# Kernel tuning notes

Hardware: AMD Instinct MI355X
Metric: run time of the kernel (lower is better)

The kernel has to match this reference:

```python
import jax, jax.numpy as jnp
import numpy as np

D_WIN = 6
SIGMA = D_WIN / 2.0  # sigma = D/2
EPS = 1e-6


def _ln(x, g, b):
    m = jnp.mean(x, -1, keepdims=True)
    v = jnp.var(x, -1, keepdims=True)
    return (x - m) / jnp.sqrt(v + EPS) * g + b


def _cross_attn(q, kv, Wq, Wkv, Wproj, bproj, nh):
    # standard multi-head cross attention, no qkv bias (qkv_bias=False)
    B, S, C = q.shape
    N = kv.shape[1]
    hd = C // nh
    scale = hd ** -0.5
    qh = (q @ Wq).reshape(B, S, nh, hd).transpose(0, 2, 1, 3) * scale
    kvh = (kv @ Wkv).reshape(B, N, 2, nh, hd).transpose(2, 0, 3, 1, 4)
    k, v = kvh[0], kvh[1]
    attn = jax.nn.softmax(jnp.einsum('bhsd,bhnd->bhsn', qh, k), -1)
    x = jnp.einsum('bhsn,bhnd->bhsd', attn, v).transpose(0, 2, 1, 3).reshape(B, S, C)
    return x @ Wproj + bproj


def setup_inputs() -> dict:
    key = jax.random.key(0)
    ks = jax.random.split(key, 32)
    B, S, C, H, W = 32, 128, 384, 8, 512

    def lin(k, i, o):
        return jax.random.normal(k, (i, o), jnp.float32) * 0.02

    inp = {
        'q': jax.random.normal(ks[0], (B, S, C), jnp.float32),
        'kv': jax.random.normal(ks[1], (B, H * W, C), jnp.float32),
        # main attention linears (qkv_bias=False)
        'Wq': lin(ks[2], C, C),
        'Wkv': lin(ks[3], C, 2 * C),
        'Wproj': lin(ks[4], C, C), 'bproj': jnp.zeros((C,), jnp.float32),
        # position predictor
        'Wp_w': lin(ks[5], C, C), 'Wp_b': jnp.zeros((C,), jnp.float32),
        'vp_w': lin(ks[6], C, 1), 'vp_b': jnp.zeros((1,), jnp.float32),
        'Wqpos': lin(ks[7], C, C), 'bqpos': jnp.zeros((C,), jnp.float32),
        # simplified RCTC decoder projection
        'Wrctc': lin(ks[8], C, C), 'brctc': jnp.zeros((C,), jnp.float32),
        # pt_to_question cross attention (2 heads)
        'ca1_Wq': lin(ks[9], C, C), 'ca1_Wkv': lin(ks[10], C, 2 * C),
        'ca1_Wproj': lin(ks[11], C, C), 'ca1_bproj': jnp.zeros((C,), jnp.float32),
        # pt_to_image cross attention (2 heads)
        'ca2_Wq': lin(ks[12], C, C), 'ca2_Wkv': lin(ks[13], C, 2 * C),
        'ca2_Wproj': lin(ks[14], C, C), 'ca2_bproj': jnp.zeros((C,), jnp.float32),
        # layernorms
        'g_q1': jnp.ones((C,), jnp.float32), 'b_q1': jnp.zeros((C,), jnp.float32),
        'g_kv1': jnp.ones((C,), jnp.float32), 'b_kv1': jnp.zeros((C,), jnp.float32),
        'g_q2': jnp.ones((C,), jnp.float32), 'b_q2': jnp.zeros((C,), jnp.float32),
        'g_kv2': jnp.ones((C,), jnp.float32), 'b_kv2': jnp.zeros((C,), jnp.float32),
        'sz_h': H, 'sz_w': W,
    }
    return inp


def reference(q, kv, Wq, Wkv, Wproj, bproj, Wp_w, Wp_b, vp_w, vp_b, Wqpos, bqpos,
              Wrctc, brctc, ca1_Wq, ca1_Wkv, ca1_Wproj, ca1_bproj,
              ca2_Wq, ca2_Wkv, ca2_Wproj, ca2_bproj,
              g_q1, b_q1, g_kv1, b_kv1, g_q2, b_q2, g_kv2, b_kv2, sz_h, sz_w):
    B, N, C = kv.shape
    S = q.shape[1]
    H, W = sz_h, sz_w
    nh = 1
    hd = C // nh
    scale = hd ** -0.5

    # RCTC decoder (simplified): (B,N,C) -> (B,C,H,W) -> collapse H -> (B,W,C) -> linear
    kv_img = kv.transpose(0, 2, 1).reshape(B, C, H, W)
    dec = kv_img.mean(axis=2).transpose(0, 2, 1)  # (B, W, C)
    dec = dec @ Wrctc + brctc

    qh = (q @ Wq).reshape(B, S, nh, hd).transpose(0, 2, 1, 3) * scale  # (B,nh,S,hd)
    kvh = (dec @ Wkv).reshape(B, W, 2, nh, hd).transpose(2, 0, 3, 1, 4)
    k, v = kvh[0], kvh[1]  # (B,nh,W,hd)

    # position prediction branch
    p = q @ Wqpos + bqpos
    p = _cross_attn(_ln(p, g_q1, b_q1), _ln(q, g_kv1, b_kv1),
                    ca1_Wq, ca1_Wkv, ca1_Wproj, ca1_bproj, 2)
    p = _cross_attn(_ln(p, g_q2, b_q2), _ln(dec, g_kv2, b_kv2),
                    ca2_Wq, ca2_Wkv, ca2_Wproj, ca2_bproj, 2)
    p_t = jax.nn.sigmoid(jnp.tanh(p @ Wp_w + Wp_b) @ vp_w + vp_b) * W  # (B,S,1)

    # Gaussian window mask around predicted position
    idx = jnp.arange(W, dtype=jnp.float32)[None, None, None, :]     # (1,1,1,W)
    pexp = p_t[:, None, :, :]                                        # (B,1,S,1)
    gauss = jnp.exp(-(idx - pexp) ** 2 / (2.0 * SIGMA ** 2))         # (B,1,S,W)

    attn = jnp.einsum('bhsd,bhwd->bhsw', qh, k) * gauss
    attn = jax.nn.softmax(attn, -1)
    x = jnp.einsum('bhsw,bhwd->bhsd', attn, v).transpose(0, 2, 1, 3).reshape(B, S, C)
    return x @ Wproj + bproj
```

## Files before the change

### kernel.cpp

```cpp
#include <hip/hip_runtime.h>
#include <hip/hip_bf16.h>
#include <math.h>

#define B_ 32
#define S_ 128
#define C_ 384
#define H_ 8
#define W_ 512
#define NKV 4096

typedef __attribute__((ext_vector_type(8))) short short8;
typedef __attribute__((ext_vector_type(4))) float floatx4;

static __device__ __forceinline__ ushort f2bf(float v) {
    __hip_bfloat16 h = __float2bfloat16(v);
    return *(ushort*)&h;
}
static __device__ __forceinline__ float ldf(const float* p, size_t i) { return p[i]; }
static __device__ __forceinline__ float ldf(const ushort* p, size_t i) {
    union { uint u; float f; } c; c.u = (uint)p[i] << 16; return c.f;
}

__global__ __launch_bounds__(256) void mean_kernel(const float* __restrict__ kv,
                                                   ushort* __restrict__ dec0b) {
    int v = blockIdx.x * blockDim.x + threadIdx.x;
    int total = B_ * W_ * (C_ / 4);
    if (v >= total) return;
    int c4  = v % (C_ / 4);
    int row = v / (C_ / 4);
    int b = row / W_;
    int w = row % W_;
    const float4* src = (const float4*)kv + (size_t)(b * NKV + w) * (C_ / 4) + c4;
    float4 s = {0.f, 0.f, 0.f, 0.f};
#pragma unroll
    for (int h = 0; h < H_; ++h) {
        float4 t = src[(size_t)h * W_ * (C_ / 4)];
        s.x += t.x; s.y += t.y; s.z += t.z; s.w += t.w;
    }
    ushort4 o;
    o.x = f2bf(s.x * 0.125f); o.y = f2bf(s.y * 0.125f);
    o.z = f2bf(s.z * 0.125f); o.w = f2bf(s.w * 0.125f);
    ((ushort4*)dec0b)[v] = o;
}

__global__ __launch_bounds__(256) void cast_kernel(const float* __restrict__ in,
                                                   ushort* __restrict__ out, int n4) {
    int v = blockIdx.x * blockDim.x + threadIdx.x;
    if (v >= n4) return;
    float4 f = ((const float4*)in)[v];
    ushort4 o;
    o.x = f2bf(f.x); o.y = f2bf(f.y); o.z = f2bf(f.z); o.w = f2bf(f.w);
    ((ushort4*)out)[v] = o;
}

struct WtDesc { const float* src[12]; ushort* dst[12]; int Kd[12]; int Nd[12]; };
__global__ __launch_bounds__(256) void wtcast_kernel(WtDesc d) {
    int wi = blockIdx.y;
    int K = d.Kd[wi], N = d.Nd[wi];
    int tiles_n = N / 32;
    int tile = blockIdx.x;
    if (tile >= (K / 32) * tiles_n) return;
    int k0 = (tile / tiles_n) * 32, n0 = (tile % tiles_n) * 32;
    __shared__ float t[32][33];
    int tid = threadIdx.x;
    int r = tid >> 3, c4 = (tid & 7) * 4;
    float4 v = *(const float4*)&d.src[wi][(size_t)(k0 + r) * N + n0 + c4];
    t[r][c4] = v.x; t[r][c4 + 1] = v.y; t[r][c4 + 2] = v.z; t[r][c4 + 3] = v.w;
    __syncthreads();
    int c = tid >> 3, k4 = (tid & 7) * 4;
    ushort4 o;
    o.x = f2bf(t[k4][c]); o.y = f2bf(t[k4 + 1][c]);
    o.z = f2bf(t[k4 + 2][c]); o.w = f2bf(t[k4 + 3][c]);
    *(ushort4*)&d.dst[wi][(size_t)(n0 + c) * K + k0 + k4] = o;
}

struct GJob {
    const ushort* A; const ushort* Bt;
    const float* bias; float* Cout; ushort* Cbf;
    int M, N, K; float alpha; int act;
};
struct GJobs { GJob j[3]; };

__global__ __launch_bounds__(256) void bgemm_kernel(GJobs gs) {
    const GJob g = gs.j[blockIdx.z];
    const int bm = blockIdx.y * 128, bn = blockIdx.x * 128;
    if (bm >= g.M || bn >= g.N) return;
    __shared__ ushort As[128 * 40];
    __shared__ ushort Bs[128 * 40];
    const int tid = threadIdx.x;
    const int wav = tid >> 6, lane = tid & 63;
    const int wm = (wav >> 1) * 64, wn = (wav & 1) * 64;
    const int lrow = lane & 15, lq = lane >> 4;

    floatx4 acc[4][4] = {};

    const int sr = tid >> 1, sc0 = (tid & 1) * 16;
    const ushort* Ag = g.A + (size_t)(bm + sr) * g.K + sc0;
    const ushort* Bg = g.Bt + (size_t)(bn + sr) * g.K + sc0;
    ushort* Asw = &As[sr * 40 + sc0];
    ushort* Bsw = &Bs[sr * 40 + sc0];

    for (int k0 = 0; k0 < g.K; k0 += 32) {
        uint4 a0 = *(const uint4*)(Ag + k0);
        uint4 a1 = *(const uint4*)(Ag + k0 + 8);
        uint4 b0 = *(const uint4*)(Bg + k0);
        uint4 b1 = *(const uint4*)(Bg + k0 + 8);
        __syncthreads();
        *(uint4*)Asw = a0; *(uint4*)(Asw + 8) = a1;
        *(uint4*)Bsw = b0; *(uint4*)(Bsw + 8) = b1;
        __syncthreads();
        short8 af[4], bfr[4];
#pragma unroll
        for (int i = 0; i < 4; ++i)
            af[i] = *(const short8*)&As[(wm + 16 * i + lrow) * 40 + lq * 8];
#pragma unroll
        for (int j = 0; j < 4; ++j)
            bfr[j] = *(const short8*)&Bs[(wn + 16 * j + lrow) * 40 + lq * 8];
#pragma unroll
        for (int i = 0; i < 4; ++i)
#pragma unroll
            for (int j = 0; j < 4; ++j)
                acc[i][j] = __builtin_amdgcn_mfma_f32_16x16x32_bf16(af[i], bfr[j], acc[i][j], 0, 0, 0);
    }

#pragma unroll
    for (int i = 0; i < 4; ++i)
#pragma unroll
        for (int j = 0; j < 4; ++j) {
            int row = bm + wm + 16 * i + lq * 4;
            int col = bn + wn + 16 * j + lrow;
            float bv = g.bias ? g.bias[col] : 0.f;
#pragma unroll
            for (int r = 0; r < 4; ++r) {
                float v = acc[i][j][r] * g.alpha + bv;
                if (g.act == 1) v = tanhf(v);
                size_t off = (size_t)(row + r) * g.N + col;
                if (g.Cout) g.Cout[off] = v;
                if (g.Cbf) g.Cbf[off] = f2bf(v);
            }
        }
}

static inline void bgemmJ(hipStream_t st, int nj, const GJob* js) {
    GJobs gs;
    int mx = 0, my = 0;
    for (int i = 0; i < nj; ++i) {
        gs.j[i] = js[i];
        int nx = js[i].N / 128, ny = js[i].M / 128;
        if (nx > mx) mx = nx;
        if (ny > my) my = ny;
    }
    for (int i = nj; i < 3; ++i) gs.j[i] = js[0];
    bgemm_kernel<<<dim3(mx, my, nj), 256, 0, st>>>(gs);
}

struct BGArgs {
    const ushort* A; const ushort* Bt;
    const float* bias; float* outF; ushort* outB;
    int lda, ldb, ldo;
    long AsB, BsB, OsB;
    int AsH, BsH, OsH;
    int K, NH;
    float alpha; int act;
};
__global__ __launch_bounds__(256) void battn_kernel(BGArgs g) {
    __shared__ ushort As[64 * 40];
    __shared__ ushort Bs[64 * 40];
    const int bn = blockIdx.x * 64, bm = blockIdx.y * 64;
    const int bat = blockIdx.z, bb = bat / g.NH, hh = bat % g.NH;
    const ushort* A  = g.A  + (size_t)bb * g.AsB + (size_t)hh * g.AsH;
    const ushort* Bt = g.Bt + (size_t)bb * g.BsB + (size_t)hh * g.BsH;
    const int tid = threadIdx.x;
    const int wav = tid >> 6, lane = tid & 63;
    const int lrow = lane & 15, lq = lane >> 4;
    const int sr = tid >> 2, sc0 = (tid & 3) * 8;
    const ushort* Ag = A  + (size_t)(bm + sr) * g.lda + sc0;
    const ushort* Bg = Bt + (size_t)(bn + sr) * g.ldb + sc0;
    ushort* Asw = &As[sr * 40 + sc0];
    ushort* Bsw = &Bs[sr * 40 + sc0];

    floatx4 acc[4] = {};

    for (int k0 = 0; k0 < g.K; k0 += 32) {
        uint4 a = *(const uint4*)(Ag + k0);
        uint4 b = *(const uint4*)(Bg + k0);
        __syncthreads();
        *(uint4*)Asw = a; *(uint4*)Bsw = b;
        __syncthreads();
        short8 af = *(const short8*)&As[(wav * 16 + lrow) * 40 + lq * 8];
#pragma unroll
        for (int j = 0; j < 4; ++j) {
            short8 bf = *(const short8*)&Bs[(16 * j + lrow) * 40 + lq * 8];
            acc[j] = __builtin_amdgcn_mfma_f32_16x16x32_bf16(af, bf, acc[j], 0, 0, 0);
        }
    }

#pragma unroll
    for (int j = 0; j < 4; ++j) {
        int col = bn + 16 * j + lrow;
        float bv = g.bias ? g.bias[col] : 0.f;
        int row0 = bm + wav * 16 + lq * 4;
#pragma unroll
        for (int r = 0; r < 4; ++r) {
            float v = acc[j][r] * g.alpha + bv;
            if (g.act == 1) v = tanhf(v);
            size_t off = (size_t)bb * g.OsB + (size_t)hh * g.OsH
                       + (size_t)(row0 + r) * g.ldo + col;
            if (g.outF) g.outF[off] = v;
            if (g.outB) g.outB[off] = f2bf(v);
        }
    }
}

static inline void battn(hipStream_t st, const ushort* A, const ushort* Bt,
                         const float* bias, float* outF, ushort* outB,
                         int M, int N, int K, float alpha, int act,
                         int lda, long AsB, int AsH,
                         int ldb, long BsB, int BsH,
                         int ldo, long OsB, int OsH,
                         int NH, int nbat) {
    BGArgs g;
    g.A = A; g.Bt = Bt; g.bias = bias; g.outF = outF; g.outB = outB;
    g.lda = lda; g.ldb = ldb; g.ldo = ldo;
    g.AsB = AsB; g.BsB = BsB; g.OsB = OsB;
    g.AsH = AsH; g.BsH = BsH; g.OsH = OsH;
    g.K = K; g.NH = NH; g.alpha = alpha; g.act = act;
    dim3 grid(N / 64, M / 64, nbat);
    battn_kernel<<<grid, 256, 0, st>>>(g);
}

static inline void bgemm64(hipStream_t st, const ushort* A, const ushort* Bt,
                           const float* bias, float* outF, ushort* outB,
                           int M, int N, int K, float alpha, int act) {
    battn(st, A, Bt, bias, outF, outB, M, N, K, alpha, act,
          K, 0, 0, K, 0, 0, N, 0, 0, 1, 1);
}

struct Ln2Desc {
    const void* X0; const float* g0; const float* b0; ushort* Y0; int bf0; int rows0;
    const void* X1; const float* g1; const float* b1; ushort* Y1; int bf1;
};
__global__ __launch_bounds__(128) void ln2_kernel(Ln2Desc d) {
    int row = blockIdx.x;
    const void* X; const float* g; const float* bb; ushort* Y; int isbf;
    if (row < d.rows0) { X = d.X0; g = d.g0; bb = d.b0; Y = d.Y0; isbf = d.bf0; }
    else { row -= d.rows0; X = d.X1; g = d.g1; bb = d.b1; Y = d.Y1; isbf = d.bf1; }
    const float*  xf = (const float*)X + (size_t)row * C_;
    const ushort* xb = (const ushort*)X + (size_t)row * C_;
    ushort* y = Y + (size_t)row * C_;
    int t = threadIdx.x;
    float v0, v1, v2;
    if (isbf) { v0 = ldf(xb, t); v1 = ldf(xb, t + 128); v2 = ldf(xb, t + 256); }
    else      { v0 = ldf(xf, t); v1 = ldf(xf, t + 128); v2 = ldf(xf, t + 256); }
    float s = v0 + v1 + v2, sq = v0 * v0 + v1 * v1 + v2 * v2;
    __shared__ float rs[128], rq[128];
    rs[t] = s; rq[t] = sq; __syncthreads();
    if (t < 64) {
        s = rs[t] + rs[t + 64]; sq = rq[t] + rq[t + 64];
        for (int o = 32; o; o >>= 1) { s += __shfl_down(s, o); sq += __shfl_down(sq, o); }
        if (t == 0) { rs[0] = s; rq[0] = sq; }
    }
    __syncthreads();
    float mean = rs[0] * (1.0f / C_);
    float var  = rq[0] * (1.0f / C_) - mean * mean;
    float inv  = rsqrtf(var + 1e-6f);
    y[t]       = f2bf((v0 - mean) * inv * g[t]       + bb[t]);
    y[t + 128] = f2bf((v1 - mean) * inv * g[t + 128] + bb[t + 128]);
    y[t + 256] = f2bf((v2 - mean) * inv * g[t + 256] + bb[t + 256]);
}

template <int NW, int GAUSS>
__global__ __launch_bounds__(256) void softmax_kernel(
    const float* __restrict__ sc, const float* __restrict__ ptv,
    ushort* __restrict__ P)
{
    int row = blockIdx.x * 4 + (threadIdx.x >> 6);
    int lane = threadIdx.x & 63;
    const float* s = sc + (size_t)row * NW;
    float pcen = GAUSS ? ptv[row] : 0.f;
    float vals[NW / 64];
    float m = -1e30f;
#pragma unroll
    for (int i = 0; i < NW / 64; ++i) {
        int w = lane + 64 * i;
        float v = s[w];
        if (GAUSS) { float dw = (float)w - pcen; v *= expf(dw * dw * (-1.0f / 18.0f)); }
        vals[i] = v; m = fmaxf(m, v);
    }
#pragma unroll
    for (int o = 32; o; o >>= 1) m = fmaxf(m, __shfl_xor(m, o));
    float sum = 0.f;
#pragma unroll
    for (int i = 0; i < NW / 64; ++i) { vals[i] = expf(vals[i] - m); sum += vals[i]; }
#pragma unroll
    for (int o = 32; o; o >>= 1) sum += __shfl_xor(sum, o);
    float rinv = 1.0f / sum;
    ushort* op = P + (size_t)row * NW;
#pragma unroll
    for (int i = 0; i < NW / 64; ++i) op[lane + 64 * i] = f2bf(vals[i] * rinv);
}

__global__ __launch_bounds__(256) void vtrans_kernel(
    const ushort* __restrict__ kvb, ushort* __restrict__ vt,
    int Nw, int C2, int CC)
{
    int b = blockIdx.z;
    int w0 = blockIdx.x * 32, c0 = blockIdx.y * 32;
    __shared__ ushort t[32][33];
    int tid = threadIdx.x;
    int wl = tid >> 3, c4 = (tid & 7) * 4;
    ushort4 v = *(const ushort4*)&kvb[((size_t)b * Nw + w0 + wl) * C2 + CC + c0 + c4];
    t[wl][c4] = v.x; t[wl][c4 + 1] = v.y; t[wl][c4 + 2] = v.z; t[wl][c4 + 3] = v.w;
    __syncthreads();
    int dl = tid >> 3, w4 = (tid & 7) * 4;
    ushort4 o;
    o.x = t[w4][dl]; o.y = t[w4 + 1][dl]; o.z = t[w4 + 2][dl]; o.w = t[w4 + 3][dl];
    *(ushort4*)&vt[((size_t)b * CC + c0 + dl) * Nw + w0 + w4] = o;
}

__global__ __launch_bounds__(128) void pt_kernel(const float* __restrict__ T,
    const float* __restrict__ vpw, const float* __restrict__ vpb,
    float* __restrict__ out) {
    int row = blockIdx.x;
    int t = threadIdx.x;
    const float* x = T + (size_t)row * C_;
    float s = x[t] * vpw[t] + x[t + 128] * vpw[t + 128] + x[t + 256] * vpw[t + 256];
    __shared__ float red[128];
    red[t] = s; __syncthreads();
    if (t < 64) {
        s = red[t] + red[t + 64];
        for (int o = 32; o; o >>= 1) s += __shfl_down(s, o);
        if (t == 0) {
            float z = s + vpb[0];
            out[row] = 512.0f / (1.0f + expf(-z));
        }
    }
}

extern "C" void kernel_launch(void* const* d_in, const int* in_sizes, int n_in,
                              void* d_out, int out_size, void* d_ws, size_t ws_size,
                              hipStream_t stream) {
    const float* q     = (const float*)d_in[0];
    const float* kv    = (const float*)d_in[1];
    const float* Wq    = (const float*)d_in[2];
    const float* Wkv   = (const float*)d_in[3];
    const float* Wproj = (const float*)d_in[4];
    const float* bproj = (const float*)d_in[5];
    const float* Wp_w  = (const float*)d_in[6];
    const float* Wp_b  = (const float*)d_in[7];
    const float* vp_w  = (const float*)d_in[8];
    const float* vp_b  = (const float*)d_in[9];
    const float* Wqpos = (const float*)d_in[10];
    const float* bqpos = (const float*)d_in[11];
    const float* Wrctc = (const float*)d_in[12];
    const float* brctc = (const float*)d_in[13];
    const float* ca1_Wq    = (const float*)d_in[14];
    const float* ca1_Wkv   = (const float*)d_in[15];
    const float* ca1_Wproj = (const float*)d_in[16];
    const float* ca1_bproj = (const float*)d_in[17];
    const float* ca2_Wq    = (const float*)d_in[18];
    const float* ca2_Wkv   = (const float*)d_in[19];
    const float* ca2_Wproj = (const float*)d_in[20];
    const float* ca2_bproj = (const float*)d_in[21];
    const float* g_q1  = (const float*)d_in[22];
    const float* b_q1  = (const float*)d_in[23];
    const float* g_kv1 = (const float*)d_in[24];
    const float* b_kv1 = (const float*)d_in[25];
    const float* g_q2  = (const float*)d_in[26];
    const float* b_q2  = (const float*)d_in[27];
    const float* g_kv2 = (const float*)d_in[28];
    const float* b_kv2 = (const float*)d_in[29];
    float* out = (float*)d_out;
    float* ws  = (float*)d_ws;

    ushort* dec0b = (ushort*)(ws);
    ushort* wb    = (ushort*)(ws + 3145728);
    ushort* qb    = (ushort*)(ws + 4251648);
    ushort* decb  = (ushort*)(ws + 5038080);
    ushort* qhb   = (ushort*)(ws + 8183808);
    float*  p     = ws + 8970240;
    ushort* pb    = (ushort*)(ws + 10543104);
    float*  t1    = ws + 11329536;
    ushort* t1b   = (ushort*)(ws + 12902400);
    ushort* t2b   = (ushort*)(ws + 13688832);
    ushort* qpb   = (ushort*)(ws + 16834560);
    ushort* kvb   = (ushort*)(ws + 17620992);
    ushort* vt    = (ushort*)(ws + 23912448);
    float*  sc    = ws + 27058176;
    ushort* Pb    = (ushort*)(ws + 31252480);
    ushort* xb    = (ushort*)(ws + 33349632);
    float*  ptb   = ws + 34136064;

    ushort* wbWq     = wb;
    ushort* wbWqpos  = wb + 147456;
    ushort* wbWrctc  = wb + 294912;
    ushort* wbC1Wq   = wb + 442368;
    ushort* wbC1Wp   = wb + 589824;
    ushort* wbC2Wq   = wb + 737280;
    ushort* wbC2Wp   = wb + 884736;
    ushort* wbWpw    = wb + 1032192;
    ushort* wbWproj  = wb + 1179648;
    ushort* wbWkv    = wb + 1327104;
    ushort* wbC1Wkv  = wb + 1622016;
    ushort* wbC2Wkv  = wb + 1916928;

    const float rs384 = 0.05103103630798288f;
    const float rs192 = 0.07216878364870323f;

    mean_kernel<<<(B_ * W_ * (C_ / 4) + 255) / 256, 256, 0, stream>>>(kv, dec0b);
    {
        WtDesc d;
        const float* s_[12] = {Wq, Wqpos, Wrctc, ca1_Wq, ca1_Wproj, ca2_Wq, ca2_Wproj,
                               Wp_w, Wproj, Wkv, ca1_Wkv, ca2_Wkv};
        ushort* t_[12] = {wbWq, wbWqpos, wbWrctc, wbC1Wq, wbC1Wp, wbC2Wq, wbC2Wp,
                          wbWpw, wbWproj, wbWkv, wbC1Wkv, wbC2Wkv};
        for (int i = 0; i < 12; ++i) {
            d.src[i] = s_[i]; d.dst[i] = t_[i];
            d.Kd[i] = 384; d.Nd[i] = (i >= 9) ? 768 : 384;
        }
        dim3 grid(288, 12);
        wtcast_kernel<<<grid, 256, 0, stream>>>(d);
        cast_kernel<<<(393216 + 255) / 256, 256, 0, stream>>>(q, qb, 393216);
    }
    {
        GJob js[3];
        js[0] = {dec0b, wbWrctc, brctc, nullptr, decb, B_ * W_, 384, 384, 1.f, 0};
        js[1] = {qb, wbWq, nullptr, nullptr, qhb, B_ * S_, 384, 384, rs384, 0};
        js[2] = {qb, wbWqpos, bqpos, p, nullptr, B_ * S_, 384, 384, 1.f, 0};
        bgemmJ(stream, 3, js);
    }
    {
        Ln2Desc d;
        d.X0 = p; d.g0 = g_q1;  d.b0 = b_q1;  d.Y0 = t1b; d.bf0 = 0; d.rows0 = B_ * S_;
        d.X1 = q; d.g1 = g_kv1; d.b1 = b_kv1; d.Y1 = t2b; d.bf1 = 0;
        ln2_kernel<<<2 * B_ * S_, 128, 0, stream>>>(d);
    }
    {
        GJob js[2];
        js[0] = {t1b, wbC1Wq, nullptr, nullptr, qpb, B_ * S_, 384, 384, rs192, 0};
        js[1] = {t2b, wbC1Wkv, nullptr, nullptr, kvb, B_ * S_, 768, 384, 1.f, 0};
        bgemmJ(stream, 2, js);
    }
    {
        dim3 gt(S_ / 32, C_ / 32, B_);
        vtrans_kernel<<<gt, 256, 0, stream>>>(kvb, vt, S_, 768, 384);
    }
    battn(stream, qpb, kvb, nullptr, sc, nullptr, 128, 128, 192, 1.f, 0,
          384, (long)S_ * 384, 192,
          768, (long)S_ * 768, 192,
          128, (long)2 * S_ * 128, S_ * 128, 2, 64);
    softmax_kernel<128, 0><<<(B_ * 2 * S_) / 4, 256, 0, stream>>>(sc, nullptr, Pb);
    battn(stream, Pb, vt, nullptr, nullptr, xb, 128, 192, 128, 1.f, 0,
          128, (long)2 * S_ * 128, S_ * 128,
          128, (long)C_ * S_, 192 * S_,
          384, (long)S_ * 384, 192, 2, 64);
    bgemm64(stream, xb, wbC1Wp, ca1_bproj, p, nullptr, B_ * S_, 384, 384, 1.f, 0);
    {
        Ln2Desc d;
        d.X0 = p;    d.g0 = g_q2;  d.b0 = b_q2;  d.Y0 = t1b; d.bf0 = 0; d.rows0 = B_ * S_;
        d.X1 = decb; d.g1 = g_kv2; d.b1 = b_kv2; d.Y1 = t2b; d.bf1 = 1;
        ln2_kernel<<<B_ * S_ + B_ * W_, 128, 0, stream>>>(d);
    }
    {
        GJob js[2];
        js[0] = {t1b, wbC2Wq, nullptr, nullptr, qpb, B_ * S_, 384, 384, rs192, 0};
        js[1] = {t2b, wbC2Wkv, nullptr, nullptr, kvb, B_ * W_, 768, 384, 1.f, 0};
        bgemmJ(stream, 2, js);
    }
    {
        dim3 gt(W_ / 32, C_ / 32, B_);
        vtrans_kernel<<<gt, 256, 0, stream>>>(kvb, vt, W_, 768, 384);
    }
    battn(stream, qpb, kvb, nullptr, sc, nullptr, 128, 512, 192, 1.f, 0,
          384, (long)S_ * 384, 192,
          768, (long)W_ * 768, 192,
          512, (long)2 * S_ * 512, S_ * 512, 2, 64);
    softmax_kernel<512, 0><<<(B_ * 2 * S_) / 4, 256, 0, stream>>>(sc, nullptr, Pb);
    battn(stream, Pb, vt, nullptr, nullptr, xb, 128, 192, 512, 1.f, 0,
          512, (long)2 * S_ * 512, S_ * 512,
          512, (long)C_ * W_, 192 * W_,
          384, (long)S_ * 384, 192, 2, 64);
    bgemm64(stream, xb, wbC2Wp, ca2_bproj, p, pb, B_ * S_, 384, 384, 1.f, 0);
    {
        GJob js[2];
        js[0] = {pb, wbWpw, Wp_b, t1, nullptr, B_ * S_, 384, 384, 1.f, 1};
        js[1] = {decb, wbWkv, nullptr, nullptr, kvb, B_ * W_, 768, 384, 1.f, 0};
        bgemmJ(stream, 2, js);
    }
    pt_kernel<<<B_ * S_, 128, 0, stream>>>(t1, vp_w, vp_b, ptb);
    {
        dim3 gt(W_ / 32, C_ / 32, B_);
        vtrans_kernel<<<gt, 256, 0, stream>>>(kvb, vt, W_, 768, 384);
    }
    battn(stream, qhb, kvb, nullptr, sc, nullptr, 128, 512, 384, 1.f, 0,
          384, (long)S_ * 384, 0,
          768, (long)W_ * 768, 0,
          512, (long)S_ * 512, 0, 1, 32);
    softmax_kernel<512, 1><<<(B_ * S_) / 4, 256, 0, stream>>>(sc, ptb, Pb);
    battn(stream, Pb, vt, nullptr, nullptr, xb, 128, 384, 512, 1.f, 0,
          512, (long)S_ * 512, 0,
          512, (long)C_ * W_, 0,
          384, (long)S_ * 384, 0, 1, 32);
    bgemm64(stream, xb, wbWproj, bproj, out, nullptr, B_ * S_, 384, 384, 1.f, 0);
}
```

Before: 586.7 us.

## Fuse V-transpose into score GEMM launches, merge prep casts, prefetch GEMM tiles

Merges the mean and q-cast kernels into one prep launch. The V-transpose kernels become extra blocks appended to the QK^T batched GEMM grid, so both run in a single launch. Both GEMM kernels now load the next K-tile from global memory into registers while the current tile is being computed (register double-buffering). Together these aim to cut launch count and hide global load latency, at the cost of a branchier kernel and more registers in use.

```diff
diff --git a/kernel.cpp b/kernel.cpp
--- a/kernel.cpp
+++ b/kernel.cpp
@@ -21,36 +21,37 @@
     union { uint u; float f; } c; c.u = (uint)p[i] << 16; return c.f;
 }
 
-__global__ __launch_bounds__(256) void mean_kernel(const float* __restrict__ kv,
-                                                   ushort* __restrict__ dec0b) {
-    int v = blockIdx.x * blockDim.x + threadIdx.x;
-    int total = B_ * W_ * (C_ / 4);
-    if (v >= total) return;
-    int c4  = v % (C_ / 4);
-    int row = v / (C_ / 4);
-    int b = row / W_;
-    int w = row % W_;
-    const float4* src = (const float4*)kv + (size_t)(b * NKV + w) * (C_ / 4) + c4;
-    float4 s = {0.f, 0.f, 0.f, 0.f};
-#pragma unroll
-    for (int h = 0; h < H_; ++h) {
-        float4 t = src[(size_t)h * W_ * (C_ / 4)];
-        s.x += t.x; s.y += t.y; s.z += t.z; s.w += t.w;
-    }
-    ushort4 o;
-    o.x = f2bf(s.x * 0.125f); o.y = f2bf(s.y * 0.125f);
-    o.z = f2bf(s.z * 0.125f); o.w = f2bf(s.w * 0.125f);
-    ((ushort4*)dec0b)[v] = o;
-}
-
-__global__ __launch_bounds__(256) void cast_kernel(const float* __restrict__ in,
-                                                   ushort* __restrict__ out, int n4) {
-    int v = blockIdx.x * blockDim.x + threadIdx.x;
-    if (v >= n4) return;
-    float4 f = ((const float4*)in)[v];
+__global__ __launch_bounds__(256) void prep_kernel(const float* __restrict__ kv,
+                                                   ushort* __restrict__ dec0b,
+                                                   const float* __restrict__ q,
+                                                   ushort* __restrict__ qb) {
+    int v = blockIdx.x * 256 + threadIdx.x;
+    const int meanTot = B_ * W_ * (C_ / 4);
+    if (v < meanTot) {
+        int c4  = v % (C_ / 4);
+        int row = v / (C_ / 4);
+        int b = row / W_;
+        int w = row % W_;
+        const float4* src = (const float4*)kv + (size_t)(b * NKV + w) * (C_ / 4) + c4;
+        float4 s = {0.f, 0.f, 0.f, 0.f};
+#pragma unroll
+        for (int h = 0; h < H_; ++h) {
+            float4 t = src[(size_t)h * W_ * (C_ / 4)];
+            s.x += t.x; s.y += t.y; s.z += t.z; s.w += t.w;
+        }
+        ushort4 o;
+        o.x = f2bf(s.x * 0.125f); o.y = f2bf(s.y * 0.125f);
+        o.z = f2bf(s.z * 0.125f); o.w = f2bf(s.w * 0.125f);
+        ((ushort4*)dec0b)[v] = o;
+        return;
+    }
+    v -= meanTot;
+    const int castTot = B_ * S_ * (C_ / 4);
+    if (v >= castTot) return;
+    float4 f = ((const float4*)q)[v];
     ushort4 o;
     o.x = f2bf(f.x); o.y = f2bf(f.y); o.z = f2bf(f.z); o.w = f2bf(f.w);
-    ((ushort4*)out)[v] = o;
+    ((ushort4*)qb)[v] = o;
 }
 
 struct WtDesc { const float* src[12]; ushort* dst[12]; int Kd[12]; int Nd[12]; };
@@ -100,15 +101,22 @@
     ushort* Asw = &As[sr * 40 + sc0];
     ushort* Bsw = &Bs[sr * 40 + sc0];
 
+    uint4 a0 = *(const uint4*)(Ag);
+    uint4 a1 = *(const uint4*)(Ag + 8);
+    uint4 b0 = *(const uint4*)(Bg);
+    uint4 b1 = *(const uint4*)(Bg + 8);
+
     for (int k0 = 0; k0 < g.K; k0 += 32) {
-        uint4 a0 = *(const uint4*)(Ag + k0);
-        uint4 a1 = *(const uint4*)(Ag + k0 + 8);
-        uint4 b0 = *(const uint4*)(Bg + k0);
-        uint4 b1 = *(const uint4*)(Bg + k0 + 8);
         __syncthreads();
         *(uint4*)Asw = a0; *(uint4*)(Asw + 8) = a1;
         *(uint4*)Bsw = b0; *(uint4*)(Bsw + 8) = b1;
         __syncthreads();
+        if (k0 + 32 < g.K) {
+            a0 = *(const uint4*)(Ag + k0 + 32);
+            a1 = *(const uint4*)(Ag + k0 + 40);
+            b0 = *(const uint4*)(Bg + k0 + 32);
+            b1 = *(const uint4*)(Bg + k0 + 40);
+        }
         short8 af[4], bfr[4];
 #pragma unroll
         for (int i = 0; i < 4; ++i)
@@ -162,15 +170,37 @@
     int AsH, BsH, OsH;
     int K, NH;
     float alpha; int act;
+    int nbat;
+    const ushort* vtsrc; ushort* vtdst; int vtNw;
 };
 __global__ __launch_bounds__(256) void battn_kernel(BGArgs g) {
     __shared__ ushort As[64 * 40];
     __shared__ ushort Bs[64 * 40];
+    const int tid = threadIdx.x;
+    const int bat = blockIdx.z;
+    if (bat >= g.nbat) {
+        int flat = (bat - g.nbat) * (gridDim.x * gridDim.y)
+                 + blockIdx.y * gridDim.x + blockIdx.x;
+        int wt_n = g.vtNw >> 5;
+        int tiles = wt_n * (C_ / 32);
+        if (flat >= B_ * tiles) return;
+        int b  = flat / tiles, rr = flat % tiles;
+        int w0 = (rr % wt_n) * 32, c0 = (rr / wt_n) * 32;
+        ushort (*t)[33] = (ushort (*)[33])As;
+        int wl = tid >> 3, c4 = (tid & 7) * 4;
+        ushort4 v = *(const ushort4*)&g.vtsrc[((size_t)b * g.vtNw + w0 + wl) * 768 + 384 + c0 + c4];
+        t[wl][c4] = v.x; t[wl][c4 + 1] = v.y; t[wl][c4 + 2] = v.z; t[wl][c4 + 3] = v.w;
+        __syncthreads();
+        int dl = tid >> 3, w4 = (tid & 7) * 4;
+        ushort4 o;
+        o.x = t[w4][dl]; o.y = t[w4 + 1][dl]; o.z = t[w4 + 2][dl]; o.w = t[w4 + 3][dl];
+        *(ushort4*)&g.vtdst[((size_t)b * C_ + c0 + dl) * g.vtNw + w0 + w4] = o;
+        return;
+    }
     const int bn = blockIdx.x * 64, bm = blockIdx.y * 64;
-    const int bat = blockIdx.z, bb = bat / g.NH, hh = bat % g.NH;
+    const int bb = bat / g.NH, hh = bat % g.NH;
     const ushort* A  = g.A  + (size_t)bb * g.AsB + (size_t)hh * g.AsH;
     const ushort* Bt = g.Bt + (size_t)bb * g.BsB + (size_t)hh * g.BsH;
-    const int tid = threadIdx.x;
     const int wav = tid >> 6, lane = tid & 63;
     const int lrow = lane & 15, lq = lane >> 4;
     const int sr = tid >> 2, sc0 = (tid & 3) * 8;
@@ -181,12 +211,17 @@
 
     floatx4 acc[4] = {};
 
+    uint4 a = *(const uint4*)(Ag);
+    uint4 b = *(const uint4*)(Bg);
+
     for (int k0 = 0; k0 < g.K; k0 += 32) {
-        uint4 a = *(const uint4*)(Ag + k0);
-        uint4 b = *(const uint4*)(Bg + k0);
         __syncthreads();
         *(uint4*)Asw = a; *(uint4*)Bsw = b;
         __syncthreads();
+        if (k0 + 32 < g.K) {
+            a = *(const uint4*)(Ag + k0 + 32);
+            b = *(const uint4*)(Bg + k0 + 32);
+        }
         short8 af = *(const short8*)&As[(wav * 16 + lrow) * 40 + lq * 8];
 #pragma unroll
         for (int j = 0; j < 4; ++j) {
@@ -218,15 +253,23 @@
                          int lda, long AsB, int AsH,
                          int ldb, long BsB, int BsH,
                          int ldo, long OsB, int OsH,
-                         int NH, int nbat) {
+                         int NH, int nbat,
+                         const ushort* vtsrc = nullptr, ushort* vtdst = nullptr,
+                         int vtNw = 0) {
     BGArgs g;
     g.A = A; g.Bt = Bt; g.bias = bias; g.outF = outF; g.outB = outB;
     g.lda = lda; g.ldb = ldb; g.ldo = ldo;
     g.AsB = AsB; g.BsB = BsB; g.OsB = OsB;
     g.AsH = AsH; g.BsH = BsH; g.OsH = OsH;
     g.K = K; g.NH = NH; g.alpha = alpha; g.act = act;
-    dim3 grid(N / 64, M / 64, nbat);
-    battn_kernel<<<grid, 256, 0, st>>>(g);
+    g.nbat = nbat; g.vtsrc = vtsrc; g.vtdst = vtdst; g.vtNw = vtNw;
+    int gx = N / 64, gy = M / 64, gz = nbat;
+    if (vtsrc) {
+        int nvt = B_ * (vtNw / 32) * (C_ / 32);
+        int per = gx * gy;
+        gz += (nvt + per - 1) / per;
+    }
+    battn_kernel<<<dim3(gx, gy, gz), 256, 0, st>>>(g);
 }
 
 static inline void bgemm64(hipStream_t st, const ushort* A, const ushort* Bt,
@@ -298,24 +341,6 @@
     ushort* op = P + (size_t)row * NW;
 #pragma unroll
     for (int i = 0; i < NW / 64; ++i) op[lane + 64 * i] = f2bf(vals[i] * rinv);
-}
-
-__global__ __launch_bounds__(256) void vtrans_kernel(
-    const ushort* __restrict__ kvb, ushort* __restrict__ vt,
-    int Nw, int C2, int CC)
-{
-    int b = blockIdx.z;
-    int w0 = blockIdx.x * 32, c0 = blockIdx.y * 32;
-    __shared__ ushort t[32][33];
-    int tid = threadIdx.x;
-    int wl = tid >> 3, c4 = (tid & 7) * 4;
-    ushort4 v = *(const ushort4*)&kvb[((size_t)b * Nw + w0 + wl) * C2 + CC + c0 + c4];
-    t[wl][c4] = v.x; t[wl][c4 + 1] = v.y; t[wl][c4 + 2] = v.z; t[wl][c4 + 3] = v.w;
-    __syncthreads();
-    int dl = tid >> 3, w4 = (tid & 7) * 4;
-    ushort4 o;
-    o.x = t[w4][dl]; o.y = t[w4 + 1][dl]; o.z = t[w4 + 2][dl]; o.w = t[w4 + 3][dl];
-    *(ushort4*)&vt[((size_t)b * CC + c0 + dl) * Nw + w0 + w4] = o;
 }
 
 __global__ __launch_bounds__(128) void pt_kernel(const float* __restrict__ T,
@@ -407,7 +432,8 @@
     const float rs384 = 0.05103103630798288f;
     const float rs192 = 0.07216878364870323f;
 
-    mean_kernel<<<(B_ * W_ * (C_ / 4) + 255) / 256, 256, 0, stream>>>(kv, dec0b);
+    prep_kernel<<<(B_ * W_ * (C_ / 4) + B_ * S_ * (C_ / 4) + 255) / 256, 256, 0, stream>>>(
+        kv, dec0b, q, qb);
     {
         WtDesc d;
         const float* s_[12] = {Wq, Wqpos, Wrctc, ca1_Wq, ca1_Wproj, ca2_Wq, ca2_Wproj,
@@ -420,7 +446,6 @@
         }
         dim3 grid(288, 12);
         wtcast_kernel<<<grid, 256, 0, stream>>>(d);
-        cast_kernel<<<(393216 + 255) / 256, 256, 0, stream>>>(q, qb, 393216);
     }
     {
         GJob js[3];
@@ -441,14 +466,11 @@
         js[1] = {t2b, wbC1Wkv, nullptr, nullptr, kvb, B_ * S_, 768, 384, 1.f, 0};
         bgemmJ(stream, 2, js);
     }
-    {
-        dim3 gt(S_ / 32, C_ / 32, B_);
-        vtrans_kernel<<<gt, 256, 0, stream>>>(kvb, vt, S_, 768, 384);
-    }
     battn(stream, qpb, kvb, nullptr, sc, nullptr, 128, 128, 192, 1.f, 0,
           384, (long)S_ * 384, 192,
           768, (long)S_ * 768, 192,
-          128, (long)2 * S_ * 128, S_ * 128, 2, 64);
+          128, (long)2 * S_ * 128, S_ * 128, 2, 64,
+          kvb, vt, S_);
     softmax_kernel<128, 0><<<(B_ * 2 * S_) / 4, 256, 0, stream>>>(sc, nullptr, Pb);
     battn(stream, Pb, vt, nullptr, nullptr, xb, 128, 192, 128, 1.f, 0,
           128, (long)2 * S_ * 128, S_ * 128,
@@ -467,14 +489,11 @@
         js[1] = {t2b, wbC2Wkv, nullptr, nullptr, kvb, B_ * W_, 768, 384, 1.f, 0};
         bgemmJ(stream, 2, js);
     }
-    {
-        dim3 gt(W_ / 32, C_ / 32, B_);
-        vtrans_kernel<<<gt, 256, 0, stream>>>(kvb, vt, W_, 768, 384);
-    }
     battn(stream, qpb, kvb, nullptr, sc, nullptr, 128, 512, 192, 1.f, 0,
           384, (long)S_ * 384, 192,
           768, (long)W_ * 768, 192,
-          512, (long)2 * S_ * 512, S_ * 512, 2, 64);
+          512, (long)2 * S_ * 512, S_ * 512, 2, 64,
+          kvb, vt, W_);
     softmax_kernel<512, 0><<<(B_ * 2 * S_) / 4, 256, 0, stream>>>(sc, nullptr, Pb);
     battn(stream, Pb, vt, nullptr, nullptr, xb, 128, 192, 512, 1.f, 0,
           512, (long)2 * S_ * 512, S_ * 512,
@@ -488,14 +507,11 @@
         bgemmJ(stream, 2, js);
     }
     pt_kernel<<<B_ * S_, 128, 0, stream>>>(t1, vp_w, vp_b, ptb);
-    {
-        dim3 gt(W_ / 32, C_ / 32, B_);
-        vtrans_kernel<<<gt, 256, 0, stream>>>(kvb, vt, W_, 768, 384);
-    }
     battn(stream, qhb, kvb, nullptr, sc, nullptr, 128, 512, 384, 1.f, 0,
           384, (long)S_ * 384, 0,
           768, (long)W_ * 768, 0,
-          512, (long)S_ * 512, 0, 1, 32);
+          512, (long)S_ * 512, 0, 1, 32,
+          kvb, vt, W_);
     softmax_kernel<512, 1><<<(B_ * S_) / 4, 256, 0, stream>>>(sc, ptb, Pb);
     battn(stream, Pb, vt, nullptr, nullptr, xb, 128, 384, 512, 1.f, 0,
           512, (long)S_ * 512, 0,
```

Result: faster. 562.4 us (-4.1%).
